# Kernel optimization log

Hardware: AMD Instinct MI355X
Metric: run time of the kernel (lower is better)

The kernel has to match this reference:

```python
import jax, jax.numpy as jnp
import numpy as np

B, L, D_MODEL, N_HEADS = 2, 2048, 1024, 16
D_HEAD = D_MODEL // N_HEADS
EPS = 1e-5


def setup_inputs() -> dict:
    key = jax.random.key(0)
    ks = jax.random.split(key, 10)
    x = jax.random.normal(ks[0], (B, L, D_MODEL), dtype=jnp.float32)
    # causal boolean mask [B, L, L]
    attn_mask = jnp.broadcast_to(jnp.tril(jnp.ones((L, L), dtype=bool)), (B, L, L))
    ts = jax.random.randint(ks[1], (B, L), 0, 10000)
    rope_lambda = jax.random.uniform(ks[2], (B, L, 1), dtype=jnp.float32)
    q_gate = jax.random.uniform(ks[3], (B, L, N_HEADS), dtype=jnp.float32)
    k_gate = jax.random.uniform(ks[4], (B, L, N_HEADS), dtype=jnp.float32)
    v_gate = jax.random.uniform(ks[5], (B, L, N_HEADS), dtype=jnp.float32)
    type_pair_bias = jax.random.normal(ks[6], (B, 1, L, L), dtype=jnp.float32)
    # parameters (torch Linear convention: y = x @ W.T + b)
    proj_w = jax.random.normal(ks[7], (4 * D_MODEL, D_MODEL), dtype=jnp.float32) * 0.02
    proj_b = jnp.zeros((4 * D_MODEL,), dtype=jnp.float32)
    out_w = jax.random.normal(ks[8], (D_MODEL, D_MODEL), dtype=jnp.float32) * 0.02
    out_b = jnp.zeros((D_MODEL,), dtype=jnp.float32)
    head_scale = jnp.ones((N_HEADS,), dtype=jnp.float32) * (D_HEAD ** -0.5)
    ln_gamma = jnp.ones((D_MODEL,), dtype=jnp.float32)
    ln_beta = jnp.zeros((D_MODEL,), dtype=jnp.float32)
    return {"x": x, "attn_mask": attn_mask, "ts": ts, "rope_lambda": rope_lambda,
            "q_gate": q_gate, "k_gate": k_gate, "v_gate": v_gate,
            "type_pair_bias": type_pair_bias, "proj_w": proj_w, "proj_b": proj_b,
            "out_w": out_w, "out_b": out_b, "head_scale": head_scale,
            "ln_gamma": ln_gamma, "ln_beta": ln_beta}


def _split_heads(t):
    b, l, _ = t.shape
    return t.reshape(b, l, N_HEADS, D_HEAD).transpose(0, 2, 1, 3)  # [B,H,L,Dh]


def _apply_rope(q, k, rope_lambda):
    # behavior-module RoPE: positions from cumsum of rope_lambda
    pos = jnp.cumsum(rope_lambda[..., 0], axis=1)  # [B, L]
    inv_freq = 1.0 / (10000.0 ** (jnp.arange(0, D_HEAD, 2, dtype=jnp.float32) / D_HEAD))
    freqs = pos[:, None, :, None] * inv_freq[None, None, None, :]  # [B,1,L,Dh/2]
    cos, sin = jnp.cos(freqs), jnp.sin(freqs)

    def rot(t):
        te, to = t[..., 0::2], t[..., 1::2]
        return jnp.concatenate([te * cos - to * sin, te * sin + to * cos], axis=-1)

    return rot(q), rot(k)


def reference(x, attn_mask, ts, rope_lambda, q_gate, k_gate, v_gate,
              type_pair_bias, proj_w, proj_b, out_w, out_b, head_scale,
              ln_gamma, ln_beta):
    b, l, d = x.shape
    h = jax.nn.silu(x @ proj_w.T + proj_b)  # [B,L,4D]
    u, v, q, k = jnp.split(h, 4, axis=-1)
    u, v, q, k = _split_heads(u), _split_heads(v), _split_heads(q), _split_heads(k)
    q, k = _apply_rope(q, k, rope_lambda)
    # multiplicative per-head gates: [B,L,H] -> [B,H,L,1]
    q = q * q_gate.transpose(0, 2, 1)[..., None]
    k = k * k_gate.transpose(0, 2, 1)[..., None]
    v = v * v_gate.transpose(0, 2, 1)[..., None]
    logits = jnp.einsum('bhid,bhjd->bhij', q, k)
    logits = logits * head_scale[None, :, None, None]
    # original does two adds: + type_pair_bias and + 3.0 * type_pair_bias
    logits = logits + type_pair_bias
    logits = logits + 3.0 * type_pair_bias
    logits = jax.nn.silu(logits)  # non-softmax SiLU attention
    logits = jnp.where(attn_mask[:, None, :, :], logits, 0.0)
    y = jnp.einsum('bhij,bhjd->bhid', logits, v)  # [B,H,L,Dh]
    y = y.transpose(0, 2, 1, 3).reshape(b, l, d)
    y = y * u.transpose(0, 2, 1, 3).reshape(b, l, d)  # gated output
    y = y @ out_w.T + out_b
    r = x + y  # dropout is identity in eval mode
    mu = jnp.mean(r, axis=-1, keepdims=True)
    var = jnp.mean((r - mu) ** 2, axis=-1, keepdims=True)
    return (r - mu) / jnp.sqrt(var + EPS) * ln_gamma + ln_beta
```

## Files before the change

### kernel.cpp

```cpp
#include <hip/hip_runtime.h>
#include <cstdint>
#include <cstddef>

typedef unsigned short u16;
typedef __attribute__((ext_vector_type(8))) short short8v;
typedef __attribute__((ext_vector_type(4))) float f32x4;

#define B_   2
#define L_   2048
#define D_   1024
#define NH_  16
#define DH_  64
#define M_   (B_*L_)
#define N4_  (4*D_)

__device__ __forceinline__ float bf2f(u16 u) {
  union { float f; unsigned int i; } v; v.i = ((unsigned int)u) << 16; return v.f;
}
__device__ __forceinline__ u16 f2bf(float f) {
  union { float f; unsigned int i; } v; v.f = f;
  unsigned int x = v.i;
  return (u16)((x + 0x7fffu + ((x >> 16) & 1u)) >> 16);
}
__device__ __forceinline__ unsigned int pk_bf16(float a, float b) {
#if __has_builtin(__builtin_amdgcn_cvt_pk_bf16_f32)
  auto r = __builtin_amdgcn_cvt_pk_bf16_f32(a, b);
  union { decltype(r) v; unsigned int u; } c; c.v = r; return c.u;
#else
  return (unsigned int)f2bf(a) | ((unsigned int)f2bf(b) << 16);
#endif
}
__device__ __forceinline__ float siluf(float x) { return x / (1.0f + __expf(-x)); }

__device__ __forceinline__ void gl2lds16(const u16* g, u16* l) {
  __builtin_amdgcn_global_load_lds(
      (const __attribute__((address_space(1))) unsigned int*)(const void*)g,
      (__attribute__((address_space(3))) unsigned int*)(void*)l,
      16, 0, 0);
}

__global__ __launch_bounds__(256) void k_conv_cum(const float* __restrict__ x,
                                                  const float* __restrict__ pw,
                                                  const float* __restrict__ ow,
                                                  const float* __restrict__ lam,
                                                  u16* __restrict__ xb,
                                                  u16* __restrict__ pwb,
                                                  u16* __restrict__ owb,
                                                  float* __restrict__ pos) {
  const int NX = M_ * D_ / 4, NP = N4_ * D_ / 4;
  int bid = blockIdx.x;
  int tid = threadIdx.x;
  if (bid < 9216) {
    int i = bid * 256 + tid;
    const float* src; u16* dst; int j;
    if (i < NX)            { src = x;  dst = xb;  j = i; }
    else if (i < NX + NP)  { src = pw; dst = pwb; j = i - NX; }
    else                   { src = ow; dst = owb; j = i - NX - NP; }
    float4 v = ((const float4*)src)[j];
    ushort4 o; o.x = f2bf(v.x); o.y = f2bf(v.y); o.z = f2bf(v.z); o.w = f2bf(v.w);
    ((ushort4*)dst)[j] = o;
  } else {
    int b = bid - 9216;
    const float* in = lam + (size_t)b * L_;
    float* out = pos + (size_t)b * L_;
    float loc[8], s = 0.0f;
#pragma unroll
    for (int i = 0; i < 8; ++i) { loc[i] = in[tid * 8 + i]; s += loc[i]; }
    __shared__ float sb[256];
    sb[tid] = s;
    __syncthreads();
    for (int off = 1; off < 256; off <<= 1) {
      float t = (tid >= off) ? sb[tid - off] : 0.0f;
      __syncthreads();
      sb[tid] += t;
      __syncthreads();
    }
    float run = sb[tid] - s;
#pragma unroll
    for (int i = 0; i < 8; ++i) { run += loc[i]; out[tid * 8 + i] = run; }
  }
}

__global__ __launch_bounds__(256) void k_gemm1(const u16* __restrict__ A,
                                               const u16* __restrict__ Bw,
                                               const float* __restrict__ bias,
                                               u16* __restrict__ hu, u16* __restrict__ hv,
                                               u16* __restrict__ hq, u16* __restrict__ hk) {
  const int K = D_;
  int bn = blockIdx.x, bm = blockIdx.y;
  int tid = threadIdx.x;
  int w = tid >> 6, lane = tid & 63, quad = lane >> 4, r16 = lane & 15;
  __shared__ __align__(16) u16 As[4096], Bs[4096];
  const u16* gA = A  + (size_t)(bm * 128 + (tid >> 2)) * K + (tid & 3) * 8;
  const u16* gB = Bw + (size_t)(bn * 128 + (tid >> 2)) * K + (tid & 3) * 8;
  f32x4 acc[4][4] = {};
  int wm = w & 1, wn = w >> 1;
  const int rowb = wm * 64, colb = wn * 64;
  for (int kt = 0; kt < K; kt += 32) {
    __syncthreads();
    gl2lds16(gA + kt,                 As + w * 512);
    gl2lds16(gA + kt + (size_t)64 * K, As + 2048 + w * 512);
    gl2lds16(gB + kt,                 Bs + w * 512);
    gl2lds16(gB + kt + (size_t)64 * K, Bs + 2048 + w * 512);
    __syncthreads();
    short8v af[4], bf[4];
#pragma unroll
    for (int mi = 0; mi < 4; ++mi)
      af[mi] = *(const short8v*)(As + (rowb + mi * 16 + r16) * 32 + quad * 8);
#pragma unroll
    for (int ni = 0; ni < 4; ++ni)
      bf[ni] = *(const short8v*)(Bs + (colb + ni * 16 + r16) * 32 + quad * 8);
#pragma unroll
    for (int mi = 0; mi < 4; ++mi)
#pragma unroll
      for (int ni = 0; ni < 4; ++ni)
        acc[mi][ni] = __builtin_amdgcn_mfma_f32_16x16x32_bf16(af[mi], bf[ni], acc[mi][ni], 0, 0, 0);
  }
  int nb = (bn * 128) >> 10;
  u16* dst = (nb == 0) ? hu : (nb == 1) ? hv : (nb == 2) ? hq : hk;
  int cbase = (bn * 128) & 1023;
  int row0 = bm * 128 + rowb;
#pragma unroll
  for (int ni = 0; ni < 4; ++ni) {
    int gcol = bn * 128 + colb + ni * 16 + r16;
    int lcol = cbase + colb + ni * 16 + r16;
    float bb = bias[gcol];
#pragma unroll
    for (int mi = 0; mi < 4; ++mi)
#pragma unroll
      for (int r = 0; r < 4; ++r) {
        int row = row0 + mi * 16 + quad * 4 + r;
        dst[(size_t)row * D_ + lcol] = f2bf(siluf(acc[mi][ni][r] + bb));
      }
  }
}

__global__ __launch_bounds__(256) void k_rope_vt(const u16* __restrict__ hq, const u16* __restrict__ hk,
                                                 const u16* __restrict__ hv,
                                                 const float* __restrict__ pos,
                                                 const float* __restrict__ qg, const float* __restrict__ kg,
                                                 const float* __restrict__ vg,
                                                 const float* __restrict__ hsc,
                                                 u16* __restrict__ Qb, u16* __restrict__ Kb,
                                                 u16* __restrict__ Vtb) {
  int bid = blockIdx.x;
  int tid = threadIdx.x;
  if (bid < 2048) {
    int idx = bid * 256 + tid;
    int j4 = idx & 7;
    int l  = (idx >> 3) & 2047;
    int bh = idx >> 14;
    int b = bh >> 4, hh = bh & 15;
    int row = b * L_ + l;
    float p = pos[row];
    float qs = qg[(size_t)row * NH_ + hh] * hsc[hh];
    float kgv = kg[(size_t)row * NH_ + hh];
    const u16* hqr = hq + (size_t)row * D_ + hh * DH_ + j4 * 8;
    const u16* hkr = hk + (size_t)row * D_ + hh * DH_ + j4 * 8;
    short8v qv = *(const short8v*)hqr;
    short8v kv = *(const short8v*)hkr;
    size_t ob = ((size_t)bh * L_ + l) * DH_ + j4 * 4;
    u16 qeo[4], qoo[4], keo[4], koo[4];
#pragma unroll
    for (int t = 0; t < 4; ++t) {
      int j = j4 * 4 + t;
      float inv = __expf(-(float)j * 0.28782313662425574f);
      float a = p * inv;
      float c, s;
      __sincosf(a, &s, &c);
      float qe = bf2f((u16)qv[2 * t]), qo = bf2f((u16)qv[2 * t + 1]);
      float ke = bf2f((u16)kv[2 * t]), ko = bf2f((u16)kv[2 * t + 1]);
      qeo[t] = f2bf((qe * c - qo * s) * qs);
      qoo[t] = f2bf((qe * s + qo * c) * qs);
      keo[t] = f2bf((ke * c - ko * s) * kgv);
      koo[t] = f2bf((ke * s + ko * c) * kgv);
    }
    *(ushort4*)(Qb + ob)      = make_ushort4(qeo[0], qeo[1], qeo[2], qeo[3]);
    *(ushort4*)(Qb + ob + 32) = make_ushort4(qoo[0], qoo[1], qoo[2], qoo[3]);
    *(ushort4*)(Kb + ob)      = make_ushort4(keo[0], keo[1], keo[2], keo[3]);
    *(ushort4*)(Kb + ob + 32) = make_ushort4(koo[0], koo[1], koo[2], koo[3]);
  } else {
    int b2 = bid - 2048;
    int lt = b2 & 31;
    int bh = b2 >> 5;
    int b = bh >> 4, hh = bh & 15;
    __shared__ u16 t[64][68];
    {
      int r = tid >> 2, cg = tid & 3;
      int row = b * L_ + lt * 64 + r;
      float gv = vg[(size_t)row * NH_ + hh];
      const u16* src = hv + (size_t)row * D_ + hh * DH_ + cg * 16;
      short8v v0 = ((const short8v*)src)[0];
      short8v v1 = ((const short8v*)src)[1];
#pragma unroll
      for (int e = 0; e < 8; ++e) {
        t[r][cg * 16 + e]     = f2bf(bf2f((u16)v0[e]) * gv);
        t[r][cg * 16 + 8 + e] = f2bf(bf2f((u16)v1[e]) * gv);
      }
    }
    __syncthreads();
    {
      int d = tid >> 2, lg = tid & 3;
      short8v o0, o1;
#pragma unroll
      for (int e = 0; e < 8; ++e) o0[e] = (short)t[lg * 16 + e][d];
#pragma unroll
      for (int e = 0; e < 8; ++e) o1[e] = (short)t[lg * 16 + 8 + e][d];
      u16* dst = Vtb + ((size_t)bh * DH_ + d) * L_ + lt * 64 + lg * 16;
      ((short8v*)dst)[0] = o0;
      ((short8v*)dst)[1] = o1;
    }
  }
}

__global__ __launch_bounds__(256, 3) void k_attn(const u16* __restrict__ Qb, const u16* __restrict__ Kb,
                                                 const u16* __restrict__ Vtb, const float* __restrict__ tpb,
                                                 const u16* __restrict__ hu, u16* __restrict__ A2) {
  int id = blockIdx.x;
  int group = id >> 5, bh = id & 31;
  int i64 = (group & 1) ? (group >> 1) : (31 - (group >> 1));
  int jmax = i64 >> 1;
  int b = bh >> 4, hh = bh & 15;
  int tid = threadIdx.x, w = tid >> 6, lane = tid & 63, quad = lane >> 4, r16 = lane & 15;
  __shared__ __align__(16) u16 Ks[8192];
  __shared__ __align__(16) u16 Vs[8192];
  __shared__ __align__(16) u16 Ps[8192];
  int wm = w & 1, wn = w >> 1;
  const u16* qtile = Qb + ((size_t)bh * L_ + (size_t)i64 * 64) * DH_;
  short8v af[2][2];
#pragma unroll
  for (int ks = 0; ks < 2; ++ks)
#pragma unroll
    for (int mi = 0; mi < 2; ++mi)
      af[ks][mi] = *(const short8v*)(qtile + (size_t)(wm * 32 + mi * 16 + r16) * DH_ + ks * 32 + quad * 8);
  f32x4 accy[4] = {};
  int li = w * 16 + r16;
  int gi = i64 * 64 + li;
  int gimax = i64 * 64 + w * 16 + 15;
  int rotr = ((r16 >> 2) & 3) << 3;
  const float* bprow = tpb + ((size_t)b * L_ + gi) * L_;
  const size_t bhbase = (size_t)bh * L_ * DH_;
#pragma unroll
  for (int s = 0; s < 4; ++s) {
    int e = tid * 8 + s * 2048;
    int sub = e >> 12, rr = (e & 4095) >> 5, kk = e & 31;
    gl2lds16(Kb + bhbase + (size_t)rr * DH_ + sub * 32 + kk, Ks + w * 512 + s * 2048);
  }
  for (int jt = 0; jt <= jmax; ++jt) {
    __syncthreads();
#pragma unroll
    for (int s = 0; s < 4; ++s)
      gl2lds16(Vtb + bhbase + (size_t)(tid >> 2) * L_ + (size_t)jt * 128 + s * 32 + (tid & 3) * 8,
               Vs + w * 512 + s * 2048);
    float4 bb[4][2];
#pragma unroll
    for (int ks = 0; ks < 4; ++ks) {
      if (jt * 128 + ks * 32 > gimax) continue;
      const float* bp = bprow + jt * 128 + ks * 32 + quad * 8;
      bb[ks][0] = ((const float4*)bp)[0];
      bb[ks][1] = ((const float4*)bp)[1];
    }
    f32x4 accs[2][4] = {};
    int limN = i64 * 64 + 63 - jt * 128 - wn * 64;
#pragma unroll
    for (int ks = 0; ks < 2; ++ks) {
#pragma unroll
      for (int ni = 0; ni < 4; ++ni) {
        if (ni * 16 > limN) continue;
        short8v bfv = *(const short8v*)(Ks + ks * 4096 + (wn * 64 + ni * 16 + r16) * 32 + quad * 8);
#pragma unroll
        for (int mi = 0; mi < 2; ++mi)
          accs[mi][ni] = __builtin_amdgcn_mfma_f32_16x16x32_bf16(af[ks][mi], bfv, accs[mi][ni], 0, 0, 0);
      }
    }
#pragma unroll
    for (int ni = 0; ni < 4; ++ni) {
      if (ni * 16 > limN) continue;
      int lj = wn * 64 + ni * 16 + r16;
      u16* pp = Ps + (lj >> 5) * 2048 + (((lj & 31) + quad * 8) & 31);
#pragma unroll
      for (int mi = 0; mi < 2; ++mi) {
        unsigned int p01 = pk_bf16(accs[mi][ni][0], accs[mi][ni][1]);
        unsigned int p23 = pk_bf16(accs[mi][ni][2], accs[mi][ni][3]);
        int li0 = (wm * 32 + mi * 16 + quad * 4) * 32;
        pp[li0]      = (u16)p01;
        pp[li0 + 32] = (u16)(p01 >> 16);
        pp[li0 + 64] = (u16)p23;
        pp[li0 + 96] = (u16)(p23 >> 16);
      }
    }
    __syncthreads();
    if (jt < jmax) {
      size_t kb2 = bhbase + (size_t)(jt + 1) * 128 * DH_;
#pragma unroll
      for (int s = 0; s < 4; ++s) {
        int e = tid * 8 + s * 2048;
        int sub = e >> 12, rr = (e & 4095) >> 5, kk = e & 31;
        gl2lds16(Kb + kb2 + (size_t)rr * DH_ + sub * 32 + kk, Ks + w * 512 + s * 2048);
      }
    }
#pragma unroll
    for (int ks = 0; ks < 4; ++ks) {
      if (jt * 128 + ks * 32 > gimax) continue;
      int colp = (quad * 8 + rotr) & 31;
      short8v sraw = *(const short8v*)(Ps + ks * 2048 + li * 32 + colp);
      int lim = gi - (jt * 128 + ks * 32 + quad * 8);
      float sv[8];
      sv[0] = siluf(fmaf(4.0f, bb[ks][0].x, bf2f((u16)sraw[0])));
      sv[1] = siluf(fmaf(4.0f, bb[ks][0].y, bf2f((u16)sraw[1])));
      sv[2] = siluf(fmaf(4.0f, bb[ks][0].z, bf2f((u16)sraw[2])));
      sv[3] = siluf(fmaf(4.0f, bb[ks][0].w, bf2f((u16)sraw[3])));
      sv[4] = siluf(fmaf(4.0f, bb[ks][1].x, bf2f((u16)sraw[4])));
      sv[5] = siluf(fmaf(4.0f, bb[ks][1].y, bf2f((u16)sraw[5])));
      sv[6] = siluf(fmaf(4.0f, bb[ks][1].z, bf2f((u16)sraw[6])));
      sv[7] = siluf(fmaf(4.0f, bb[ks][1].w, bf2f((u16)sraw[7])));
#pragma unroll
      for (int j = 0; j < 8; ++j) if (j > lim) sv[j] = 0.0f;
      union { short8v v; unsigned int u[4]; } pa;
      pa.u[0] = pk_bf16(sv[0], sv[1]);
      pa.u[1] = pk_bf16(sv[2], sv[3]);
      pa.u[2] = pk_bf16(sv[4], sv[5]);
      pa.u[3] = pk_bf16(sv[6], sv[7]);
      short8v vb[4];
#pragma unroll
      for (int ni = 0; ni < 4; ++ni)
        vb[ni] = *(const short8v*)(Vs + ks * 2048 + (ni * 16 + r16) * 32 + quad * 8);
#pragma unroll
      for (int ni = 0; ni < 4; ++ni)
        accy[ni] = __builtin_amdgcn_mfma_f32_16x16x32_bf16(pa.v, vb[ni], accy[ni], 0, 0, 0);
    }
  }
#pragma unroll
  for (int ni = 0; ni < 4; ++ni) {
    int d = ni * 16 + r16;
#pragma unroll
    for (int r = 0; r < 4; ++r) {
      int lr = w * 16 + quad * 4 + r;
      size_t rowg = (size_t)b * L_ + (size_t)i64 * 64 + lr;
      float u = bf2f(hu[rowg * D_ + hh * DH_ + d]);
      A2[rowg * D_ + hh * DH_ + d] = f2bf(accy[ni][r] * u);
    }
  }
}

__global__ __launch_bounds__(256) void k_gemm2(const u16* __restrict__ A,
                                               const u16* __restrict__ Bw,
                                               const float* __restrict__ bias,
                                               const float* __restrict__ xres,
                                               float* __restrict__ out) {
  const int K = D_;
  int bn = blockIdx.x, bm = blockIdx.y;
  int tid = threadIdx.x;
  int w = tid >> 6, lane = tid & 63, quad = lane >> 4, r16 = lane & 15;
  __shared__ __align__(16) u16 As[4096], Bs[4096];
  const u16* gA = A  + (size_t)(bm * 128 + (tid >> 2)) * K + (tid & 3) * 8;
  const u16* gB = Bw + (size_t)(bn * 128 + (tid >> 2)) * K + (tid & 3) * 8;
  f32x4 acc[4][4] = {};
  int wm = w & 1, wn = w >> 1;
  const int rowb = wm * 64, colb = wn * 64;
  for (int kt = 0; kt < K; kt += 32) {
    __syncthreads();
    gl2lds16(gA + kt,                  As + w * 512);
    gl2lds16(gA + kt + (size_t)64 * K, As + 2048 + w * 512);
    gl2lds16(gB + kt,                  Bs + w * 512);
    gl2lds16(gB + kt + (size_t)64 * K, Bs + 2048 + w * 512);
    __syncthreads();
    short8v af[4], bf[4];
#pragma unroll
    for (int mi = 0; mi < 4; ++mi)
      af[mi] = *(const short8v*)(As + (rowb + mi * 16 + r16) * 32 + quad * 8);
#pragma unroll
    for (int ni = 0; ni < 4; ++ni)
      bf[ni] = *(const short8v*)(Bs + (colb + ni * 16 + r16) * 32 + quad * 8);
#pragma unroll
    for (int mi = 0; mi < 4; ++mi)
#pragma unroll
      for (int ni = 0; ni < 4; ++ni)
        acc[mi][ni] = __builtin_amdgcn_mfma_f32_16x16x32_bf16(af[mi], bf[ni], acc[mi][ni], 0, 0, 0);
  }
  int row0 = bm * 128 + rowb, col0 = bn * 128 + colb;
#pragma unroll
  for (int ni = 0; ni < 4; ++ni) {
    int col = col0 + ni * 16 + r16;
    float bb = bias[col];
#pragma unroll
    for (int mi = 0; mi < 4; ++mi)
#pragma unroll
      for (int r = 0; r < 4; ++r) {
        int row = row0 + mi * 16 + quad * 4 + r;
        out[(size_t)row * D_ + col] = acc[mi][ni][r] + bb + xres[(size_t)row * D_ + col];
      }
  }
}

__global__ __launch_bounds__(256) void k_ln(float* __restrict__ r,
                                            const float* __restrict__ g,
                                            const float* __restrict__ be) {
  int row = blockIdx.x, tid = threadIdx.x;
  float* pr = r + (size_t)row * D_;
  __shared__ float s1[4], s2[4];
  float v[4];
#pragma unroll
  for (int i = 0; i < 4; ++i) v[i] = pr[i * 256 + tid];
  float s = v[0] + v[1] + v[2] + v[3];
#pragma unroll
  for (int o = 32; o > 0; o >>= 1) s += __shfl_down(s, o, 64);
  if ((tid & 63) == 0) s1[tid >> 6] = s;
  __syncthreads();
  float mu = (s1[0] + s1[1] + s1[2] + s1[3]) * (1.0f / D_);
  float d = 0.0f;
#pragma unroll
  for (int i = 0; i < 4; ++i) { float t = v[i] - mu; d += t * t; }
#pragma unroll
  for (int o = 32; o > 0; o >>= 1) d += __shfl_down(d, o, 64);
  if ((tid & 63) == 0) s2[tid >> 6] = d;
  __syncthreads();
  float var = (s2[0] + s2[1] + s2[2] + s2[3]) * (1.0f / D_);
  float inv = rsqrtf(var + 1e-5f);
#pragma unroll
  for (int i = 0; i < 4; ++i) {
    int c = i * 256 + tid;
    pr[c] = (v[i] - mu) * inv * g[c] + be[c];
  }
}

extern "C" void kernel_launch(void* const* d_in, const int* in_sizes, int n_in,
                              void* d_out, int out_size, void* d_ws, size_t ws_size,
                              hipStream_t stream) {
  const float* x   = (const float*)d_in[0];
  const float* lam = (const float*)d_in[3];
  const float* qg  = (const float*)d_in[4];
  const float* kg  = (const float*)d_in[5];
  const float* vg  = (const float*)d_in[6];
  const float* tpb = (const float*)d_in[7];
  const float* pw  = (const float*)d_in[8];
  const float* pb  = (const float*)d_in[9];
  const float* ow  = (const float*)d_in[10];
  const float* ob  = (const float*)d_in[11];
  const float* hsc = (const float*)d_in[12];
  const float* lng = (const float*)d_in[13];
  const float* lnb = (const float*)d_in[14];
  float* out = (float*)d_out;

  char* ws = (char*)d_ws;
  u16* xb   = (u16*)(ws + 0);
  u16* pwb  = (u16*)(ws + 8388608);
  u16* owb  = (u16*)(ws + 16777216);
  u16* hu   = (u16*)(ws + 18874368);
  u16* hv   = (u16*)(ws + 27262976);
  u16* hq   = (u16*)(ws + 35651584);
  u16* hk   = (u16*)(ws + 44040192);
  float* pos = (float*)(ws + 52428800);
  u16* Qb  = xb;
  u16* Kb  = pwb;
  u16* Vtb = hq;
  u16* A2  = hk;

  k_conv_cum<<<9218, 256, 0, stream>>>(x, pw, ow, lam, xb, pwb, owb, pos);
  k_gemm1<<<dim3(32, 32), 256, 0, stream>>>(xb, pwb, pb, hu, hv, hq, hk);
  k_rope_vt<<<3072, 256, 0, stream>>>(hq, hk, hv, pos, qg, kg, vg, hsc, Qb, Kb, Vtb);
  k_attn<<<1024, 256, 0, stream>>>(Qb, Kb, Vtb, tpb, hu, A2);
  k_gemm2<<<dim3(8, 32), 256, 0, stream>>>(A2, owb, ob, x, out);
  k_ln<<<4096, 256, 0, stream>>>(out, lng, lnb);
}
```

Before: 321.5 us.

## Double-buffer GEMM tiles, swizzle LDS, and fuse bias/SiLU into attention score MFMA

Both GEMM kernels now keep two LDS stages, issuing the next K-slice's global-to-LDS loads before computing on the current one. This removes one barrier per iteration and is meant to overlap memory with MFMA. All LDS tiles use an XOR-like rotation swizzle to reduce bank conflicts, and the GEMMs declare launch bounds with 4 blocks per CU. The attention kernel computes scores transposed with the bias preloaded into the accumulator, then applies SiLU and the causal mask directly in registers before writing bf16 probabilities to a padded LDS buffer. This drops the separate raw-score round trip through LDS, at the cost of more LDS and register pressure.

After: 330.8 us. 1.03x slower.

```diff
diff --git a/kernel.cpp b/kernel.cpp
--- a/kernel.cpp
+++ b/kernel.cpp
@@ -81,35 +81,53 @@
   }
 }
 
-__global__ __launch_bounds__(256) void k_gemm1(const u16* __restrict__ A,
-                                               const u16* __restrict__ Bw,
-                                               const float* __restrict__ bias,
-                                               u16* __restrict__ hu, u16* __restrict__ hv,
-                                               u16* __restrict__ hq, u16* __restrict__ hk) {
+__global__ __launch_bounds__(256, 4) void k_gemm1(const u16* __restrict__ A,
+                                                  const u16* __restrict__ Bw,
+                                                  const float* __restrict__ bias,
+                                                  u16* __restrict__ hu, u16* __restrict__ hv,
+                                                  u16* __restrict__ hq, u16* __restrict__ hk) {
   const int K = D_;
-  int bn = blockIdx.x, bm = blockIdx.y;
-  int tid = threadIdx.x;
+  int bn = blockIdx.x, bm = blockIdx.y, tid = threadIdx.x;
   int w = tid >> 6, lane = tid & 63, quad = lane >> 4, r16 = lane & 15;
-  __shared__ __align__(16) u16 As[4096], Bs[4096];
-  const u16* gA = A  + (size_t)(bm * 128 + (tid >> 2)) * K + (tid & 3) * 8;
-  const u16* gB = Bw + (size_t)(bn * 128 + (tid >> 2)) * K + (tid & 3) * 8;
+  __shared__ __align__(16) u16 As[8192], Bs[8192];
+  const u16* gA = A  + (size_t)(bm * 128) * K;
+  const u16* gB = Bw + (size_t)(bn * 128) * K;
+  int srow = tid >> 2, sc = tid & 3;
+#pragma unroll
+  for (int s = 0; s < 2; ++s) {
+    int row = s * 64 + srow;
+    int q = (sc - (row >> 1)) & 3;
+    gl2lds16(gA + (size_t)row * K + q * 8, As + s * 2048 + w * 512);
+    gl2lds16(gB + (size_t)row * K + q * 8, Bs + s * 2048 + w * 512);
+  }
   f32x4 acc[4][4] = {};
   int wm = w & 1, wn = w >> 1;
   const int rowb = wm * 64, colb = wn * 64;
-  for (int kt = 0; kt < K; kt += 32) {
-    __syncthreads();
-    gl2lds16(gA + kt,                 As + w * 512);
-    gl2lds16(gA + kt + (size_t)64 * K, As + 2048 + w * 512);
-    gl2lds16(gB + kt,                 Bs + w * 512);
-    gl2lds16(gB + kt + (size_t)64 * K, Bs + 2048 + w * 512);
-    __syncthreads();
+  for (int n = 0; n < 32; ++n) {
+    __syncthreads();
+    if (n + 1 < 32) {
+      int kt = (n + 1) * 32, pb = (n + 1) & 1;
+#pragma unroll
+      for (int s = 0; s < 2; ++s) {
+        int row = s * 64 + srow;
+        int q = (sc - (row >> 1)) & 3;
+        gl2lds16(gA + (size_t)row * K + kt + q * 8, As + pb * 4096 + s * 2048 + w * 512);
+        gl2lds16(gB + (size_t)row * K + kt + q * 8, Bs + pb * 4096 + s * 2048 + w * 512);
+      }
+    }
+    const u16* Ab = As + (n & 1) * 4096;
+    const u16* Bb = Bs + (n & 1) * 4096;
     short8v af[4], bf[4];
 #pragma unroll
-    for (int mi = 0; mi < 4; ++mi)
-      af[mi] = *(const short8v*)(As + (rowb + mi * 16 + r16) * 32 + quad * 8);
-#pragma unroll
-    for (int ni = 0; ni < 4; ++ni)
-      bf[ni] = *(const short8v*)(Bs + (colb + ni * 16 + r16) * 32 + quad * 8);
+    for (int mi = 0; mi < 4; ++mi) {
+      int row = rowb + mi * 16 + r16;
+      af[mi] = *(const short8v*)(Ab + (row * 4 + ((quad + (row >> 1)) & 3)) * 8);
+    }
+#pragma unroll
+    for (int ni = 0; ni < 4; ++ni) {
+      int row = colb + ni * 16 + r16;
+      bf[ni] = *(const short8v*)(Bb + (row * 4 + ((quad + (row >> 1)) & 3)) * 8);
+    }
 #pragma unroll
     for (int mi = 0; mi < 4; ++mi)
 #pragma unroll
@@ -222,112 +240,93 @@
   int jmax = i64 >> 1;
   int b = bh >> 4, hh = bh & 15;
   int tid = threadIdx.x, w = tid >> 6, lane = tid & 63, quad = lane >> 4, r16 = lane & 15;
+  int wj = w & 1, wi = w >> 1;
   __shared__ __align__(16) u16 Ks[8192];
   __shared__ __align__(16) u16 Vs[8192];
-  __shared__ __align__(16) u16 Ps[8192];
-  int wm = w & 1, wn = w >> 1;
-  const u16* qtile = Qb + ((size_t)bh * L_ + (size_t)i64 * 64) * DH_;
-  short8v af[2][2];
+  __shared__ __align__(16) u16 Ps[8704];
+  const size_t bhbase = (size_t)bh * L_ * DH_;
+  int gibase = i64 * 64 + wi * 32;
+  const u16* qt = Qb + bhbase + (size_t)gibase * DH_;
+  short8v bq[2][2];
 #pragma unroll
   for (int ks = 0; ks < 2; ++ks)
 #pragma unroll
-    for (int mi = 0; mi < 2; ++mi)
-      af[ks][mi] = *(const short8v*)(qtile + (size_t)(wm * 32 + mi * 16 + r16) * DH_ + ks * 32 + quad * 8);
+    for (int ti = 0; ti < 2; ++ti)
+      bq[ks][ti] = *(const short8v*)(qt + (size_t)(ti * 16 + r16) * DH_ + ks * 32 + quad * 8);
+#pragma unroll
+  for (int s = 0; s < 4; ++s) {
+    int row = (s & 1) * 64 + (tid >> 2);
+    int q = ((tid & 3) - (row >> 1)) & 3;
+    gl2lds16(Kb + bhbase + (size_t)row * DH_ + (s >> 1) * 32 + q * 8, Ks + s * 2048 + w * 512);
+  }
   f32x4 accy[4] = {};
-  int li = w * 16 + r16;
-  int gi = i64 * 64 + li;
-  int gimax = i64 * 64 + w * 16 + 15;
-  int rotr = ((r16 >> 2) & 3) << 3;
-  const float* bprow = tpb + ((size_t)b * L_ + gi) * L_;
-  const size_t bhbase = (size_t)bh * L_ * DH_;
-#pragma unroll
-  for (int s = 0; s < 4; ++s) {
-    int e = tid * 8 + s * 2048;
-    int sub = e >> 12, rr = (e & 4095) >> 5, kk = e & 31;
-    gl2lds16(Kb + bhbase + (size_t)rr * DH_ + sub * 32 + kk, Ks + w * 512 + s * 2048);
-  }
+  int gimax_w = i64 * 64 + w * 16 + 15;
   for (int jt = 0; jt <= jmax; ++jt) {
     __syncthreads();
 #pragma unroll
-    for (int s = 0; s < 4; ++s)
-      gl2lds16(Vtb + bhbase + (size_t)(tid >> 2) * L_ + (size_t)jt * 128 + s * 32 + (tid & 3) * 8,
-               Vs + w * 512 + s * 2048);
-    float4 bb[4][2];
+    for (int s = 0; s < 4; ++s) {
+      int row = tid >> 2;
+      int q = ((tid & 3) - (row >> 1)) & 3;
+      gl2lds16(Vtb + bhbase + (size_t)row * L_ + jt * 128 + s * 32 + q * 8, Vs + s * 2048 + w * 512);
+    }
+#pragma unroll
+    for (int tj = 0; tj < 4; ++tj) {
+      int jlo = jt * 128 + wj * 64 + tj * 16;
+      bool anyM = jlo <= gibase + 31;
+      short8v ak0, ak1;
+      if (anyM) {
+        int row = wj * 64 + tj * 16 + r16;
+        int sw = (quad + (row >> 1)) & 3;
+        ak0 = *(const short8v*)(Ks + (row * 4 + sw) * 8);
+        ak1 = *(const short8v*)(Ks + 4096 + (row * 4 + sw) * 8);
+      }
+#pragma unroll
+      for (int ti = 0; ti < 2; ++ti) {
+        int gmaxt = gibase + ti * 16 + 15;
+        bool doM = jlo <= gmaxt;
+        bool doW = (jlo & ~31) <= gmaxt;
+        if (!doW) continue;
+        unsigned int p01 = 0, p23 = 0;
+        if (doM) {
+          int gi = gibase + ti * 16 + r16;
+          float4 bv = *(const float4*)(tpb + ((size_t)b * L_ + gi) * L_ + jlo + quad * 4);
+          f32x4 acc;
+          acc[0] = 4.0f * bv.x; acc[1] = 4.0f * bv.y; acc[2] = 4.0f * bv.z; acc[3] = 4.0f * bv.w;
+          acc = __builtin_amdgcn_mfma_f32_16x16x32_bf16(ak0, bq[0][ti], acc, 0, 0, 0);
+          acc = __builtin_amdgcn_mfma_f32_16x16x32_bf16(ak1, bq[1][ti], acc, 0, 0, 0);
+          int j0 = jlo + quad * 4;
+          float v0 = (j0     <= gi) ? siluf(acc[0]) : 0.0f;
+          float v1 = (j0 + 1 <= gi) ? siluf(acc[1]) : 0.0f;
+          float v2 = (j0 + 2 <= gi) ? siluf(acc[2]) : 0.0f;
+          float v3 = (j0 + 3 <= gi) ? siluf(acc[3]) : 0.0f;
+          p01 = pk_bf16(v0, v1);
+          p23 = pk_bf16(v2, v3);
+        }
+        int iloc = wi * 32 + ti * 16 + r16;
+        int jloc = wj * 64 + tj * 16 + quad * 4;
+        *(uint2*)(Ps + iloc * 136 + jloc) = make_uint2(p01, p23);
+      }
+    }
+    __syncthreads();
+    if (jt < jmax) {
+      const size_t kb = bhbase + (size_t)(jt + 1) * 128 * DH_;
+#pragma unroll
+      for (int s = 0; s < 4; ++s) {
+        int row = (s & 1) * 64 + (tid >> 2);
+        int q = ((tid & 3) - (row >> 1)) & 3;
+        gl2lds16(Kb + kb + (size_t)row * DH_ + (s >> 1) * 32 + q * 8, Ks + s * 2048 + w * 512);
+      }
+    }
 #pragma unroll
     for (int ks = 0; ks < 4; ++ks) {
-      if (jt * 128 + ks * 32 > gimax) continue;
-      const float* bp = bprow + jt * 128 + ks * 32 + quad * 8;
-      bb[ks][0] = ((const float4*)bp)[0];
-      bb[ks][1] = ((const float4*)bp)[1];
-    }
-    f32x4 accs[2][4] = {};
-    int limN = i64 * 64 + 63 - jt * 128 - wn * 64;
-#pragma unroll
-    for (int ks = 0; ks < 2; ++ks) {
+      if (jt * 128 + ks * 32 > gimax_w) continue;
+      short8v pa = *(const short8v*)(Ps + (w * 16 + r16) * 136 + ks * 32 + quad * 8);
 #pragma unroll
       for (int ni = 0; ni < 4; ++ni) {
-        if (ni * 16 > limN) continue;
-        short8v bfv = *(const short8v*)(Ks + ks * 4096 + (wn * 64 + ni * 16 + r16) * 32 + quad * 8);
-#pragma unroll
-        for (int mi = 0; mi < 2; ++mi)
-          accs[mi][ni] = __builtin_amdgcn_mfma_f32_16x16x32_bf16(af[ks][mi], bfv, accs[mi][ni], 0, 0, 0);
-      }
-    }
-#pragma unroll
-    for (int ni = 0; ni < 4; ++ni) {
-      if (ni * 16 > limN) continue;
-      int lj = wn * 64 + ni * 16 + r16;
-      u16* pp = Ps + (lj >> 5) * 2048 + (((lj & 31) + quad * 8) & 31);
-#pragma unroll
-      for (int mi = 0; mi < 2; ++mi) {
-        unsigned int p01 = pk_bf16(accs[mi][ni][0], accs[mi][ni][1]);
-        unsigned int p23 = pk_bf16(accs[mi][ni][2], accs[mi][ni][3]);
-        int li0 = (wm * 32 + mi * 16 + quad * 4) * 32;
-        pp[li0]      = (u16)p01;
-        pp[li0 + 32] = (u16)(p01 >> 16);
-        pp[li0 + 64] = (u16)p23;
-        pp[li0 + 96] = (u16)(p23 >> 16);
-      }
-    }
-    __syncthreads();
-    if (jt < jmax) {
-      size_t kb2 = bhbase + (size_t)(jt + 1) * 128 * DH_;
-#pragma unroll
-      for (int s = 0; s < 4; ++s) {
-        int e = tid * 8 + s * 2048;
-        int sub = e >> 12, rr = (e & 4095) >> 5, kk = e & 31;
-        gl2lds16(Kb + kb2 + (size_t)rr * DH_ + sub * 32 + kk, Ks + w * 512 + s * 2048);
-      }
-    }
-#pragma unroll
-    for (int ks = 0; ks < 4; ++ks) {
-      if (jt * 128 + ks * 32 > gimax) continue;
-      int colp = (quad * 8 + rotr) & 31;
-      short8v sraw = *(const short8v*)(Ps + ks * 2048 + li * 32 + colp);
-      int lim = gi - (jt * 128 + ks * 32 + quad * 8);
-      float sv[8];
-      sv[0] = siluf(fmaf(4.0f, bb[ks][0].x, bf2f((u16)sraw[0])));
-      sv[1] = siluf(fmaf(4.0f, bb[ks][0].y, bf2f((u16)sraw[1])));
-      sv[2] = siluf(fmaf(4.0f, bb[ks][0].z, bf2f((u16)sraw[2])));
-      sv[3] = siluf(fmaf(4.0f, bb[ks][0].w, bf2f((u16)sraw[3])));
-      sv[4] = siluf(fmaf(4.0f, bb[ks][1].x, bf2f((u16)sraw[4])));
-      sv[5] = siluf(fmaf(4.0f, bb[ks][1].y, bf2f((u16)sraw[5])));
-      sv[6] = siluf(fmaf(4.0f, bb[ks][1].z, bf2f((u16)sraw[6])));
-      sv[7] = siluf(fmaf(4.0f, bb[ks][1].w, bf2f((u16)sraw[7])));
-#pragma unroll
-      for (int j = 0; j < 8; ++j) if (j > lim) sv[j] = 0.0f;
-      union { short8v v; unsigned int u[4]; } pa;
-      pa.u[0] = pk_bf16(sv[0], sv[1]);
-      pa.u[1] = pk_bf16(sv[2], sv[3]);
-      pa.u[2] = pk_bf16(sv[4], sv[5]);
-      pa.u[3] = pk_bf16(sv[6], sv[7]);
-      short8v vb[4];
-#pragma unroll
-      for (int ni = 0; ni < 4; ++ni)
-        vb[ni] = *(const short8v*)(Vs + ks * 2048 + (ni * 16 + r16) * 32 + quad * 8);
-#pragma unroll
-      for (int ni = 0; ni < 4; ++ni)
-        accy[ni] = __builtin_amdgcn_mfma_f32_16x16x32_bf16(pa.v, vb[ni], accy[ni], 0, 0, 0);
+        int row = ni * 16 + r16;
+        short8v vb = *(const short8v*)(Vs + ks * 2048 + (row * 4 + ((quad + (row >> 1)) & 3)) * 8);
+        accy[ni] = __builtin_amdgcn_mfma_f32_16x16x32_bf16(pa, vb, accy[ni], 0, 0, 0);
+      }
     }
   }
 #pragma unroll
@@ -343,35 +342,53 @@
   }
 }
 
-__global__ __launch_bounds__(256) void k_gemm2(const u16* __restrict__ A,
-                                               const u16* __restrict__ Bw,
-                                               const float* __restrict__ bias,
-                                               const float* __restrict__ xres,
-                                               float* __restrict__ out) {
+__global__ __launch_bounds__(256, 4) void k_gemm2(const u16* __restrict__ A,
+                                                  const u16* __restrict__ Bw,
+                                                  const float* __restrict__ bias,
+                                                  const float* __restrict__ xres,
+                                                  float* __restrict__ out) {
   const int K = D_;
-  int bn = blockIdx.x, bm = blockIdx.y;
-  int tid = threadIdx.x;
+  int bn = blockIdx.x, bm = blockIdx.y, tid = threadIdx.x;
   int w = tid >> 6, lane = tid & 63, quad = lane >> 4, r16 = lane & 15;
-  __shared__ __align__(16) u16 As[4096], Bs[4096];
-  const u16* gA = A  + (size_t)(bm * 128 + (tid >> 2)) * K + (tid & 3) * 8;
-  const u16* gB = Bw + (size_t)(bn * 128 + (tid >> 2)) * K + (tid & 3) * 8;
+  __shared__ __align__(16) u16 As[8192], Bs[8192];
+  const u16* gA = A  + (size_t)(bm * 128) * K;
+  const u16* gB = Bw + (size_t)(bn * 128) * K;
+  int srow = tid >> 2, sc = tid & 3;
+#pragma unroll
+  for (int s = 0; s < 2; ++s) {
+    int row = s * 64 + srow;
+    int q = (sc - (row >> 1)) & 3;
+    gl2lds16(gA + (size_t)row * K + q * 8, As + s * 2048 + w * 512);
+    gl2lds16(gB + (size_t)row * K + q * 8, Bs + s * 2048 + w * 512);
+  }
   f32x4 acc[4][4] = {};
   int wm = w & 1, wn = w >> 1;
   const int rowb = wm * 64, colb = wn * 64;
-  for (int kt = 0; kt < K; kt += 32) {
-    __syncthreads();
-    gl2lds16(gA + kt,                  As + w * 512);
-    gl2lds16(gA + kt + (size_t)64 * K, As + 2048 + w * 512);
-    gl2lds16(gB + kt,                  Bs + w * 512);
-    gl2lds16(gB + kt + (size_t)64 * K, Bs + 2048 + w * 512);
-    __syncthreads();
+  for (int n = 0; n < 32; ++n) {
+    __syncthreads();
+    if (n + 1 < 32) {
+      int kt = (n + 1) * 32, pb = (n + 1) & 1;
+#pragma unroll
+      for (int s = 0; s < 2; ++s) {
+        int row = s * 64 + srow;
+        int q = (sc - (row >> 1)) & 3;
+        gl2lds16(gA + (size_t)row * K + kt + q * 8, As + pb * 4096 + s * 2048 + w * 512);
+        gl2lds16(gB + (size_t)row * K + kt + q * 8, Bs + pb * 4096 + s * 2048 + w * 512);
+      }
+    }
+    const u16* Ab = As + (n & 1) * 4096;
+    const u16* Bb = Bs + (n & 1) * 4096;
     short8v af[4], bf[4];
 #pragma unroll
-    for (int mi = 0; mi < 4; ++mi)
-      af[mi] = *(const short8v*)(As + (rowb + mi * 16 + r16) * 32 + quad * 8);
-#pragma unroll
-    for (int ni = 0; ni < 4; ++ni)
-      bf[ni] = *(const short8v*)(Bs + (colb + ni * 16 + r16) * 32 + quad * 8);
+    for (int mi = 0; mi < 4; ++mi) {
+      int row = rowb + mi * 16 + r16;
+      af[mi] = *(const short8v*)(Ab + (row * 4 + ((quad + (row >> 1)) & 3)) * 8);
+    }
+#pragma unroll
+    for (int ni = 0; ni < 4; ++ni) {
+      int row = colb + ni * 16 + r16;
+      bf[ni] = *(const short8v*)(Bb + (row * 4 + ((quad + (row >> 1)) & 3)) * 8);
+    }
 #pragma unroll
     for (int mi = 0; mi < 4; ++mi)
 #pragma unroll
```
